# Kernel optimization log

Hardware: AMD Instinct MI355X
Metric: run time of the kernel (lower is better)

Reference implementation:

```python
import jax, jax.numpy as jnp
import numpy as np

KN = 4        # kernel_number
K = 3         # kernel size
CIN = 256
COUT = 256
BN_EPS = 1e-5


def _rotation_matrices(thetas):
    """thetas: [b, n] -> rot mats [b, n, 9, 9] (faithful port of _get_rotation_matrix)."""
    b, n = thetas.shape
    t = thetas.reshape(-1)                      # [b*n]
    x = jnp.cos(t); y = jnp.sin(t)
    a = x - y; bxy = x * y; c = x + y
    z = jnp.zeros_like(t); o = jnp.ones_like(t)
    pos = [
        [a, 1 - a, z, z, z, z, z, z, z],
        [z, x - bxy, bxy, z, 1 - c + bxy, y - bxy, z, z, z],
        [z, z, a, z, z, 1 - a, z, z, z],
        [bxy, y - bxy, z, x - bxy, 1 - c + bxy, z, z, z, z],
        [z, z, z, z, o, z, z, z, z],
        [z, z, z, z, 1 - c + bxy, x - bxy, z, y - bxy, bxy],
        [z, z, z, 1 - a, z, z, a, z, z],
        [z, z, z, y - bxy, 1 - c + bxy, z, bxy, x - bxy, z],
        [z, z, z, z, z, z, z, 1 - a, a],
    ]
    neg = [
        [c, z, z, 1 - c, z, z, z, z, z],
        [-bxy, x + bxy, z, bxy - y, 1 - a - bxy, z, z, z, z],
        [z, 1 - c, c, z, z, z, z, z, z],
        [z, z, z, x + bxy, 1 - a - bxy, z, -bxy, bxy - y, z],
        [z, z, z, z, o, z, z, z, z],
        [z, bxy - y, -bxy, z, 1 - a - bxy, x + bxy, z, z, z],
        [z, z, z, z, z, z, c, 1 - c, z],
        [z, z, z, z, 1 - a - bxy, bxy - y, z, x + bxy, -bxy],
        [z, z, z, z, z, 1 - c, z, z, c],
    ]
    P = jnp.stack([jnp.stack(r, 0) for r in pos], 0)    # [9, 9, b*n]
    N = jnp.stack([jnp.stack(r, 0) for r in neg], 0)    # [9, 9, b*n]
    R = jnp.where(t >= 0, P, N)                          # [9, 9, b*n]
    return R.transpose(2, 0, 1).reshape(b, n, K * K, K * K)


def _rotate_weights(weights, lambdas, thetas):
    """weights [n, Cout, Cin, 3, 3], lambdas/thetas [b, n] -> [b*Cout, Cin, 3, 3]."""
    b, n = thetas.shape
    _, Cout, Cin, _, _ = weights.shape
    rot = _rotation_matrices(thetas) * lambdas[:, :, None, None]   # [b, n, 9, 9]
    rot = rot.transpose(0, 2, 1, 3).reshape(b * K * K, n * K * K)  # [b*9, n*9]
    w = weights.transpose(0, 3, 4, 1, 2).reshape(n * K * K, Cout * Cin)
    w = rot @ w                                                    # [b*9, Cout*Cin]
    w = w.reshape(b, K, K, Cout, Cin).transpose(0, 3, 4, 1, 2)
    return w.reshape(b * Cout, Cin, K, K)


def _forward(x, weight, w_lambda, w_theta, bn_gamma, bn_beta, bn_mean, bn_var):
    b, Cin, H, W = x.shape
    Cout = weight.shape[1]
    # routing: GAP -> linear heads (sigmoid for lambdas, softsign*pi for thetas)
    pooled = x.mean(axis=(2, 3))                        # [b, Cin]
    lambdas = jax.nn.sigmoid(pooled @ w_lambda)         # [b, n]
    thetas = jax.nn.soft_sign(pooled @ w_theta) * jnp.pi  # [b, n]
    # per-sample rotated weights + grouped conv (groups = b)
    rw = _rotate_weights(weight, lambdas, thetas)       # [b*Cout, Cin, 3, 3]
    xr = x.reshape(1, b * Cin, H, W)
    out = jax.lax.conv_general_dilated(
        xr, rw, window_strides=(1, 1), padding=((1, 1), (1, 1)),
        dimension_numbers=('NCHW', 'OIHW', 'NCHW'), feature_group_count=b)
    out = out.reshape(b, Cout, H, W)
    # BatchNorm (inference, running stats) + ReLU
    inv = jax.lax.rsqrt(bn_var + BN_EPS)
    out = (out - bn_mean[None, :, None, None]) * (inv * bn_gamma)[None, :, None, None] \
          + bn_beta[None, :, None, None]
    return jax.nn.relu(out)


def setup_inputs() -> dict:
    key = jax.random.key(0)
    ks = jax.random.split(key, 8)
    B, H, W = 16, 64, 64
    x = jax.random.normal(ks[0], (B, CIN, H, W), dtype=jnp.float32)
    fan_in = CIN * K * K
    weight = jax.random.normal(ks[1], (KN, COUT, CIN, K, K), dtype=jnp.float32) * np.sqrt(2.0 / fan_in)
    w_lambda = jax.random.normal(ks[2], (CIN, KN), dtype=jnp.float32) * np.sqrt(2.0 / CIN)
    w_theta = jax.random.normal(ks[3], (CIN, KN), dtype=jnp.float32) * np.sqrt(2.0 / CIN)
    bn_gamma = jax.random.uniform(ks[4], (COUT,), dtype=jnp.float32, minval=0.5, maxval=1.5)
    bn_beta = jax.random.normal(ks[5], (COUT,), dtype=jnp.float32) * 0.1
    bn_mean = jax.random.normal(ks[6], (COUT,), dtype=jnp.float32) * 0.1
    bn_var = jax.random.uniform(ks[7], (COUT,), dtype=jnp.float32, minval=0.5, maxval=1.5)
    return {'x': x, 'weight': weight, 'w_lambda': w_lambda, 'w_theta': w_theta,
            'bn_gamma': bn_gamma, 'bn_beta': bn_beta, 'bn_mean': bn_mean, 'bn_var': bn_var}


def reference(x, weight, w_lambda, w_theta, bn_gamma, bn_beta, bn_mean, bn_var):
    return _forward(x, weight, w_lambda, w_theta, bn_gamma, bn_beta, bn_mean, bn_var)
```

## Files before the change

### kernel.cpp

```cpp
#include <hip/hip_runtime.h>
#include <math.h>

typedef __bf16  bf16x8 __attribute__((ext_vector_type(8)));
typedef float   f32x4  __attribute__((ext_vector_type(4)));

#define GLD_LDS16(dst, src)                                                      \
    __builtin_amdgcn_global_load_lds(                                            \
        (const __attribute__((address_space(1))) unsigned int*)(src),            \
        (__attribute__((address_space(3))) unsigned int*)(dst), 16, 0, 0)

__global__ __launch_bounds__(256) void transpose_kernel(const float* __restrict__ x,
                                                        __bf16* __restrict__ xT) {
    int h = blockIdx.x, b = blockIdx.y;
    int lane = threadIdx.x & 63, wv = threadIdx.x >> 6;
#pragma unroll
    for (int i = 0; i < 8; i++) {
        int cq = i * 4 + wv;
        const float* src = x + (((size_t)(b * 256 + cq * 8) * 64 + h) * 64 + lane);
        bf16x8 o;
#pragma unroll
        for (int j = 0; j < 8; j++) o[j] = (__bf16)src[(size_t)j * 4096];
        *(bf16x8*)(xT + (((size_t)(b * 64 + h) * 64 + lane) * 256 + cq * 8)) = o;
    }
}

__global__ __launch_bounds__(256) void pool_kernel(const float* __restrict__ x,
                                                   float* __restrict__ pooled) {
    int bc = blockIdx.x;
    const float* p = x + (size_t)bc * 4096;
    int t = threadIdx.x;
    float s = 0.f;
#pragma unroll
    for (int i = 0; i < 16; i++) s += p[t + i * 256];
#pragma unroll
    for (int off = 32; off > 0; off >>= 1) s += __shfl_down(s, off, 64);
    __shared__ float red[4];
    if ((t & 63) == 0) red[t >> 6] = s;
    __syncthreads();
    if (t == 0) pooled[bc] = (red[0] + red[1] + red[2] + red[3]) * (1.f / 4096.f);
}

__global__ __launch_bounds__(256) void rotw_kernel(
    const float* __restrict__ weight, const float* __restrict__ pooled,
    const float* __restrict__ w_lambda, const float* __restrict__ w_theta,
    __bf16* __restrict__ rwq) {
    __shared__ __attribute__((aligned(16))) float sl[16][4][9][12];
    __shared__ float wlds[4][2304];
    int co = blockIdx.x;
    int t = threadIdx.x;
#pragma unroll
    for (int n = 0; n < 4; n++) {
        const float* wp = weight + ((size_t)n * 256 + co) * 2304;
        for (int i = t; i < 2304; i += 256) wlds[n][i] = wp[i];
    }
    if (t < 64) {
        int b = t >> 2, n = t & 3;
        float zl = 0.f, zt = 0.f;
        for (int ci = 0; ci < 256; ci++) {
            float p = pooled[b * 256 + ci];
            zl += p * w_lambda[ci * 4 + n];
            zt += p * w_theta[ci * 4 + n];
        }
        float lam = 1.f / (1.f + expf(-zl));
        float th  = 3.14159265358979323846f * (zt / (1.f + fabsf(zt)));
        float xc = cosf(th), ys = sinf(th);
        float a = xc - ys, bb = xc * ys, c = xc + ys;
        float R[9][9];
#pragma unroll
        for (int i = 0; i < 9; i++)
#pragma unroll
            for (int j = 0; j < 9; j++) R[i][j] = 0.f;
        if (th >= 0.f) {
            R[0][0] = a;       R[0][1] = 1 - a;
            R[1][1] = xc - bb; R[1][2] = bb;       R[1][4] = 1 - c + bb; R[1][5] = ys - bb;
            R[2][2] = a;       R[2][5] = 1 - a;
            R[3][0] = bb;      R[3][1] = ys - bb;  R[3][3] = xc - bb;    R[3][4] = 1 - c + bb;
            R[4][4] = 1.f;
            R[5][4] = 1 - c + bb; R[5][5] = xc - bb; R[5][7] = ys - bb;  R[5][8] = bb;
            R[6][3] = 1 - a;   R[6][6] = a;
            R[7][3] = ys - bb; R[7][4] = 1 - c + bb; R[7][6] = bb;       R[7][7] = xc - bb;
            R[8][7] = 1 - a;   R[8][8] = a;
        } else {
            R[0][0] = c;       R[0][3] = 1 - c;
            R[1][0] = -bb;     R[1][1] = xc + bb;  R[1][3] = bb - ys;    R[1][4] = 1 - a - bb;
            R[2][1] = 1 - c;   R[2][2] = c;
            R[3][3] = xc + bb; R[3][4] = 1 - a - bb; R[3][6] = -bb;      R[3][7] = bb - ys;
            R[4][4] = 1.f;
            R[5][1] = bb - ys; R[5][2] = -bb;      R[5][4] = 1 - a - bb; R[5][5] = xc + bb;
            R[6][6] = c;       R[6][7] = 1 - c;
            R[7][4] = 1 - a - bb; R[7][5] = bb - ys; R[7][7] = xc + bb;  R[7][8] = -bb;
            R[8][5] = 1 - c;   R[8][8] = c;
        }
#pragma unroll
        for (int p = 0; p < 9; p++) {
#pragma unroll
            for (int q = 0; q < 9; q++) sl[b][n][p][q] = lam * R[p][q];
            sl[b][n][p][9] = sl[b][n][p][10] = sl[b][n][p][11] = 0.f;
        }
    }
    __syncthreads();
    int ci = t;
    float4 wa[4], wb[4];
    float  wc[4];
#pragma unroll
    for (int n = 0; n < 4; n++) {
        const float* wp = &wlds[n][ci * 9];
        wa[n] = make_float4(wp[0], wp[1], wp[2], wp[3]);
        wb[n] = make_float4(wp[4], wp[5], wp[6], wp[7]);
        wc[n] = wp[8];
    }
    for (int b = 0; b < 16; b++) {
#pragma unroll
        for (int p = 0; p < 9; p++) {
            float s = 0.f;
#pragma unroll
            for (int n = 0; n < 4; n++) {
                float4 sa = *(const float4*)&sl[b][n][p][0];
                float4 sb = *(const float4*)&sl[b][n][p][4];
                float  sc = sl[b][n][p][8];
                s += sa.x * wa[n].x + sa.y * wa[n].y + sa.z * wa[n].z + sa.w * wa[n].w
                   + sb.x * wb[n].x + sb.y * wb[n].y + sb.z * wb[n].z + sb.w * wb[n].w
                   + sc * wc[n];
            }
            rwq[(((size_t)b * 9 + p) * 256 + co) * 256 + ci] = (__bf16)s;
        }
    }
}

__global__ __launch_bounds__(256, 2) void conv_kernel(
    const __bf16* __restrict__ xT, const __bf16* __restrict__ rwq,
    const float* __restrict__ bn_gamma, const float* __restrict__ bn_beta,
    const float* __restrict__ bn_mean,  const float* __restrict__ bn_var,
    float* __restrict__ out) {
    __shared__ __attribute__((aligned(16))) __bf16 xs[10][4][66][8];
    __shared__ __attribute__((aligned(16))) __bf16 as9[9][4][66][8];
    __shared__ float bns[64], bnh[64];

    const int t    = threadIdx.x;
    const int lane = t & 63;
    const int wv   = t >> 6;
    const int l15  = lane & 15;
    const int kq4  = lane >> 4;

    const int lin  = blockIdx.x;
    const int r    = lin & 7;
    const int k    = lin >> 3;
    const int b    = (r << 1) | (k >> 5);
    const int inner = k & 31;
    const int co0  = (inner & 3) << 6;
    const int h0   = (inner >> 2) << 3;

    if (t < 64) {
        float inv = rsqrtf(bn_var[co0 + t] + 1e-5f);
        float sc = bn_gamma[co0 + t] * inv;
        bns[t] = sc;
        bnh[t] = bn_beta[co0 + t] - bn_mean[co0 + t] * sc;
    }

    f32x4 acc[2][4][4];
#pragma unroll
    for (int rr = 0; rr < 2; rr++)
#pragma unroll
        for (int m = 0; m < 4; m++)
#pragma unroll
            for (int n = 0; n < 4; n++) acc[rr][m][n] = (f32x4){0.f, 0.f, 0.f, 0.f};

    const uint4 zero4 = {0u, 0u, 0u, 0u};
    if (t < 40) {
        int rr = t >> 2, kq = t & 3;
        *(uint4*)&xs[rr][kq][0][0]  = zero4;
        *(uint4*)&xs[rr][kq][65][0] = zero4;
    }

    for (int ci0 = 0; ci0 < 256; ci0 += 32) {
        __syncthreads();
#pragma unroll
        for (int u = wv * 10; u < wv * 10 + 10; u++) {
            int rr = u >> 2, kq = u & 3;
            int hh = h0 - 1 + rr;
            if (hh >= 0 && hh < 64) {
                const __bf16* src = xT + (((size_t)(b * 64 + hh) * 64 + lane) * 256 + ci0 + kq * 8);
                GLD_LDS16(&xs[rr][kq][1 + lane][0], src);
            } else {
                *(uint4*)&xs[rr][kq][1 + lane][0] = zero4;
            }
        }
#pragma unroll
        for (int u = wv * 9; u < wv * 9 + 9; u++) {
            int tap = u >> 2, kq = u & 3;
            const __bf16* src = rwq +
                ((((size_t)b * 9 + tap) * 256 + co0 + lane) * 256 + ci0 + kq * 8);
            GLD_LDS16(&as9[tap][kq][lane][0], src);
        }
        __syncthreads();
#pragma unroll
        for (int tap = 0; tap < 9; tap++) {
            const int dh = tap / 3, dw = tap % 3;
            bf16x8 af[4];
#pragma unroll
            for (int m = 0; m < 4; m++)
                af[m] = *(const bf16x8*)&as9[tap][kq4][m * 16 + l15][0];
#pragma unroll
            for (int rr = 0; rr < 2; rr++) {
                const int hl = wv + rr * 4;
#pragma unroll
                for (int nt = 0; nt < 4; nt++) {
                    bf16x8 bfr = *(const bf16x8*)&xs[hl + dh][kq4][nt * 16 + l15 + dw][0];
#pragma unroll
                    for (int m = 0; m < 4; m++)
                        acc[rr][m][nt] = __builtin_amdgcn_mfma_f32_16x16x32_bf16(
                            af[m], bfr, acc[rr][m][nt], 0, 0, 0);
                }
            }
        }
    }

#pragma unroll
    for (int rr = 0; rr < 2; rr++) {
        const int h = h0 + wv + rr * 4;
#pragma unroll
        for (int m = 0; m < 4; m++) {
#pragma unroll
            for (int reg = 0; reg < 4; reg++) {
                int col = m * 16 + kq4 * 4 + reg;
                float sc = bns[col], sh = bnh[col];
                int co = co0 + col;
#pragma unroll
                for (int nt = 0; nt < 4; nt++) {
                    int w = nt * 16 + l15;
                    float v = acc[rr][m][nt][reg] * sc + sh;
                    out[(((size_t)b * 256 + co) * 64 + h) * 64 + w] = v > 0.f ? v : 0.f;
                }
            }
        }
    }
}

extern "C" void kernel_launch(void* const* d_in, const int* in_sizes, int n_in,
                              void* d_out, int out_size, void* d_ws, size_t ws_size,
                              hipStream_t stream) {
    const float* x        = (const float*)d_in[0];
    const float* weight   = (const float*)d_in[1];
    const float* w_lambda = (const float*)d_in[2];
    const float* w_theta  = (const float*)d_in[3];
    const float* bn_gamma = (const float*)d_in[4];
    const float* bn_beta  = (const float*)d_in[5];
    const float* bn_mean  = (const float*)d_in[6];
    const float* bn_var   = (const float*)d_in[7];
    float* out = (float*)d_out;

    char* ws = (char*)d_ws;
    float*  pooled  = (float*)(ws);
    __bf16* xT      = (__bf16*)(ws + 49152);
    __bf16* rwq     = (__bf16*)(ws + 49152 + 33554432);

    transpose_kernel<<<dim3(64, 16), 256, 0, stream>>>(x, xT);
    pool_kernel<<<4096, 256, 0, stream>>>(x, pooled);
    rotw_kernel<<<256, 256, 0, stream>>>(weight, pooled, w_lambda, w_theta, rwq);
    conv_kernel<<<512, 256, 0, stream>>>(xT, rwq,
                                         bn_gamma, bn_beta, bn_mean, bn_var, out);
}
```

Before: 269.0 us.

## Double-buffer conv input tiles, load weights from global, pool from bf16 transpose

The conv kernel now uses 512-thread blocks covering 16 output rows and double-buffers the input tile in LDS, prefetching the next channel chunk while computing. Weight fragments are read straight from global memory instead of being staged in LDS. Pooling reads the smaller bf16 transposed tensor and reduces with atomics, with zeroing done in the transpose kernel. The risks are more global weight traffic per tap, pooled means computed from bf16-rounded inputs, and halving the grid to one block per CU.

```diff
diff --git a/kernel.cpp b/kernel.cpp
--- a/kernel.cpp
+++ b/kernel.cpp
@@ -10,7 +10,11 @@
         (__attribute__((address_space(3))) unsigned int*)(dst), 16, 0, 0)
 
 __global__ __launch_bounds__(256) void transpose_kernel(const float* __restrict__ x,
-                                                        __bf16* __restrict__ xT) {
+                                                        __bf16* __restrict__ xT,
+                                                        float* __restrict__ pooled) {
+    if (blockIdx.x == 0 && blockIdx.y == 0) {
+        for (int i = threadIdx.x; i < 4096; i += 256) pooled[i] = 0.f;
+    }
     int h = blockIdx.x, b = blockIdx.y;
     int lane = threadIdx.x & 63, wv = threadIdx.x >> 6;
 #pragma unroll
@@ -24,20 +28,36 @@
     }
 }
 
-__global__ __launch_bounds__(256) void pool_kernel(const float* __restrict__ x,
+__global__ __launch_bounds__(256) void pool_kernel(const __bf16* __restrict__ xT,
                                                    float* __restrict__ pooled) {
-    int bc = blockIdx.x;
-    const float* p = x + (size_t)bc * 4096;
+    int blk = blockIdx.x;
+    int b = blk >> 4, s = blk & 15;
     int t = threadIdx.x;
-    float s = 0.f;
-#pragma unroll
-    for (int i = 0; i < 16; i++) s += p[t + i * 256];
-#pragma unroll
-    for (int off = 32; off > 0; off >>= 1) s += __shfl_down(s, off, 64);
-    __shared__ float red[4];
-    if ((t & 63) == 0) red[t >> 6] = s;
+    int oc  = (t & 31) << 3;
+    int hw0 = t >> 5;
+    float a8[8];
+#pragma unroll
+    for (int j = 0; j < 8; j++) a8[j] = 0.f;
+    const __bf16* base = xT + (((size_t)b * 4096 + s * 256 + hw0) * 256) + oc;
+#pragma unroll 4
+    for (int i = 0; i < 32; ++i) {
+        bf16x8 v = *(const bf16x8*)(base + (size_t)i * 8 * 256);
+#pragma unroll
+        for (int j = 0; j < 8; j++) a8[j] += (float)v[j];
+    }
+    __shared__ float red[256][8];
+#pragma unroll
+    for (int j = 0; j < 8; j++) red[t][j] = a8[j];
     __syncthreads();
-    if (t == 0) pooled[bc] = (red[0] + red[1] + red[2] + red[3]) * (1.f / 4096.f);
+    if (t < 32) {
+#pragma unroll
+        for (int j = 0; j < 8; j++) {
+            float s8 = 0.f;
+#pragma unroll
+            for (int g = 0; g < 8; g++) s8 += red[g * 32 + t][j];
+            atomicAdd(&pooled[b * 256 + t * 8 + j], s8 * (1.f / 4096.f));
+        }
+    }
 }
 
 __global__ __launch_bounds__(256) void rotw_kernel(
@@ -127,13 +147,26 @@
     }
 }
 
-__global__ __launch_bounds__(256, 2) void conv_kernel(
+#define STAGE_X(bufsel, ci0_)                                                     \
+    _Pragma("unroll")                                                             \
+    for (int u = wv * 9; u < wv * 9 + 9; ++u) {                                   \
+        int rr_ = u >> 2, kq_ = u & 3;                                            \
+        int hh_ = h0 - 1 + rr_;                                                   \
+        if (hh_ >= 0 && hh_ < 64) {                                               \
+            const __bf16* src_ = xT + (((size_t)(b * 64 + hh_) * 64 + lane) * 256 \
+                                       + (ci0_) + kq_ * 8);                       \
+            GLD_LDS16(&xs[bufsel][rr_][kq_][1 + lane][0], src_);                  \
+        } else {                                                                  \
+            *(uint4*)&xs[bufsel][rr_][kq_][1 + lane][0] = zero4;                  \
+        }                                                                         \
+    }
+
+__global__ __launch_bounds__(512) void conv_kernel(
     const __bf16* __restrict__ xT, const __bf16* __restrict__ rwq,
     const float* __restrict__ bn_gamma, const float* __restrict__ bn_beta,
     const float* __restrict__ bn_mean,  const float* __restrict__ bn_var,
     float* __restrict__ out) {
-    __shared__ __attribute__((aligned(16))) __bf16 xs[10][4][66][8];
-    __shared__ __attribute__((aligned(16))) __bf16 as9[9][4][66][8];
+    __shared__ __attribute__((aligned(16))) __bf16 xs[2][18][4][66][8];
     __shared__ float bns[64], bnh[64];
 
     const int t    = threadIdx.x;
@@ -145,10 +178,10 @@
     const int lin  = blockIdx.x;
     const int r    = lin & 7;
     const int k    = lin >> 3;
-    const int b    = (r << 1) | (k >> 5);
-    const int inner = k & 31;
+    const int b    = (r << 1) | (k >> 4);
+    const int inner = k & 15;
     const int co0  = (inner & 3) << 6;
-    const int h0   = (inner >> 2) << 3;
+    const int h0   = (inner >> 2) << 4;
 
     if (t < 64) {
         float inv = rsqrtf(bn_var[co0 + t] + 1e-5f);
@@ -157,6 +190,16 @@
         bnh[t] = bn_beta[co0 + t] - bn_mean[co0 + t] * sc;
     }
 
+    const uint4 zero4 = {0u, 0u, 0u, 0u};
+    if (t < 288) {
+        int side = t & 1;
+        int kq = (t >> 1) & 3;
+        int rem = t >> 3;
+        int rr = rem % 18;
+        int bf = rem / 18;
+        *(uint4*)&xs[bf][rr][kq][side * 65][0] = zero4;
+    }
+
     f32x4 acc[2][4][4];
 #pragma unroll
     for (int rr = 0; rr < 2; rr++)
@@ -165,47 +208,28 @@
 #pragma unroll
             for (int n = 0; n < 4; n++) acc[rr][m][n] = (f32x4){0.f, 0.f, 0.f, 0.f};
 
-    const uint4 zero4 = {0u, 0u, 0u, 0u};
-    if (t < 40) {
-        int rr = t >> 2, kq = t & 3;
-        *(uint4*)&xs[rr][kq][0][0]  = zero4;
-        *(uint4*)&xs[rr][kq][65][0] = zero4;
-    }
-
-    for (int ci0 = 0; ci0 < 256; ci0 += 32) {
-        __syncthreads();
-#pragma unroll
-        for (int u = wv * 10; u < wv * 10 + 10; u++) {
-            int rr = u >> 2, kq = u & 3;
-            int hh = h0 - 1 + rr;
-            if (hh >= 0 && hh < 64) {
-                const __bf16* src = xT + (((size_t)(b * 64 + hh) * 64 + lane) * 256 + ci0 + kq * 8);
-                GLD_LDS16(&xs[rr][kq][1 + lane][0], src);
-            } else {
-                *(uint4*)&xs[rr][kq][1 + lane][0] = zero4;
-            }
-        }
-#pragma unroll
-        for (int u = wv * 9; u < wv * 9 + 9; u++) {
-            int tap = u >> 2, kq = u & 3;
-            const __bf16* src = rwq +
-                ((((size_t)b * 9 + tap) * 256 + co0 + lane) * 256 + ci0 + kq * 8);
-            GLD_LDS16(&as9[tap][kq][lane][0], src);
-        }
-        __syncthreads();
+    STAGE_X(0, 0);
+    __syncthreads();
+
+    for (int c = 0; c < 8; ++c) {
+        const int cur = c & 1;
+        const int ci0 = c << 5;
+        if (c < 7) { STAGE_X(cur ^ 1, ci0 + 32); }
 #pragma unroll
         for (int tap = 0; tap < 9; tap++) {
             const int dh = tap / 3, dw = tap % 3;
             bf16x8 af[4];
 #pragma unroll
             for (int m = 0; m < 4; m++)
-                af[m] = *(const bf16x8*)&as9[tap][kq4][m * 16 + l15][0];
+                af[m] = *(const bf16x8*)(rwq +
+                    ((((size_t)b * 9 + tap) * 256 + co0 + m * 16 + l15) * 256
+                     + ci0 + kq4 * 8));
 #pragma unroll
             for (int rr = 0; rr < 2; rr++) {
-                const int hl = wv + rr * 4;
+                const int hl = wv * 2 + rr;
 #pragma unroll
                 for (int nt = 0; nt < 4; nt++) {
-                    bf16x8 bfr = *(const bf16x8*)&xs[hl + dh][kq4][nt * 16 + l15 + dw][0];
+                    bf16x8 bfr = *(const bf16x8*)&xs[cur][hl + dh][kq4][nt * 16 + l15 + dw][0];
 #pragma unroll
                     for (int m = 0; m < 4; m++)
                         acc[rr][m][nt] = __builtin_amdgcn_mfma_f32_16x16x32_bf16(
@@ -213,11 +237,12 @@
                 }
             }
         }
+        __syncthreads();
     }
 
 #pragma unroll
     for (int rr = 0; rr < 2; rr++) {
-        const int h = h0 + wv + rr * 4;
+        const int h = h0 + wv * 2 + rr;
 #pragma unroll
         for (int m = 0; m < 4; m++) {
 #pragma unroll
@@ -254,9 +279,9 @@
     __bf16* xT      = (__bf16*)(ws + 49152);
     __bf16* rwq     = (__bf16*)(ws + 49152 + 33554432);
 
-    transpose_kernel<<<dim3(64, 16), 256, 0, stream>>>(x, xT);
-    pool_kernel<<<4096, 256, 0, stream>>>(x, pooled);
+    transpose_kernel<<<dim3(64, 16), 256, 0, stream>>>(x, xT, pooled);
+    pool_kernel<<<256, 256, 0, stream>>>(xT, pooled);
     rotw_kernel<<<256, 256, 0, stream>>>(weight, pooled, w_lambda, w_theta, rwq);
-    conv_kernel<<<512, 256, 0, stream>>>(xT, rwq,
+    conv_kernel<<<256, 512, 0, stream>>>(xT, rwq,
                                          bn_gamma, bn_beta, bn_mean, bn_var, out);
 }
```

Result: slower. 343.0 us (+27.5%).

## Stage transpose through LDS, pool from bf16 copy, hoist routing into own kernel

Applied to the files above, without the earlier changes.

The transpose kernel now reads x with coalesced float4 loads, packs channel pairs into LDS and writes contiguous 16-byte chunks of xT. The pool kernel now reduces the half-size bf16 xT instead of rereading the fp32 input, and accumulates into pooled with atomics after the transpose kernel zeroes it. The routing computation (lambda/theta and the rotation matrices) moves into a single small kernel, so the 256 rotw blocks no longer each recompute it serially. The aim is to cut global memory traffic and redundant serial work. The cost is pooling from bf16-rounded values, plus one extra launch and atomics.

```diff
diff --git a/kernel.cpp b/kernel.cpp
--- a/kernel.cpp
+++ b/kernel.cpp
@@ -10,39 +10,128 @@
         (__attribute__((address_space(3))) unsigned int*)(dst), 16, 0, 0)
 
 __global__ __launch_bounds__(256) void transpose_kernel(const float* __restrict__ x,
-                                                        __bf16* __restrict__ xT) {
-    int h = blockIdx.x, b = blockIdx.y;
-    int lane = threadIdx.x & 63, wv = threadIdx.x >> 6;
-#pragma unroll
-    for (int i = 0; i < 8; i++) {
-        int cq = i * 4 + wv;
-        const float* src = x + (((size_t)(b * 256 + cq * 8) * 64 + h) * 64 + lane);
-        bf16x8 o;
-#pragma unroll
-        for (int j = 0; j < 8; j++) o[j] = (__bf16)src[(size_t)j * 4096];
-        *(bf16x8*)(xT + (((size_t)(b * 64 + h) * 64 + lane) * 256 + cq * 8)) = o;
-    }
-}
-
-__global__ __launch_bounds__(256) void pool_kernel(const float* __restrict__ x,
+                                                        __bf16* __restrict__ xT,
+                                                        float* __restrict__ pooled) {
+    __shared__ unsigned int lp[128][68];
+    const int h = blockIdx.x, b = blockIdx.y;
+    const int t = threadIdx.x;
+    if (h == 0 && b == 0) {
+        for (int i = t; i < 4096; i += 256) pooled[i] = 0.f;
+    }
+    const int w4 = t & 15;
+#pragma unroll
+    for (int k = 0; k < 8; ++k) {
+        int ci2 = k * 16 + (t >> 4);
+        int ci  = ci2 * 2;
+        const float4 a = *(const float4*)(x + (((size_t)(b * 256 + ci    ) * 64 + h) * 64 + w4 * 4));
+        const float4 c = *(const float4*)(x + (((size_t)(b * 256 + ci + 1) * 64 + h) * 64 + w4 * 4));
+        union { __bf16 hh[2]; unsigned int u; } p0, p1, p2, p3;
+        p0.hh[0] = (__bf16)a.x; p0.hh[1] = (__bf16)c.x;
+        p1.hh[0] = (__bf16)a.y; p1.hh[1] = (__bf16)c.y;
+        p2.hh[0] = (__bf16)a.z; p2.hh[1] = (__bf16)c.z;
+        p3.hh[0] = (__bf16)a.w; p3.hh[1] = (__bf16)c.w;
+        uint4 v = {p0.u, p1.u, p2.u, p3.u};
+        *(uint4*)&lp[ci2][w4 * 4] = v;
+    }
+    __syncthreads();
+    const int w = t >> 2, q = t & 3;
+    __bf16* dst = xT + (((size_t)b * 64 + h) * 64 + w) * 256 + q * 64;
+#pragma unroll
+    for (int j = 0; j < 8; ++j) {
+        int c0 = q * 32 + j * 4;
+        uint4 v;
+        v.x = lp[c0 + 0][w];
+        v.y = lp[c0 + 1][w];
+        v.z = lp[c0 + 2][w];
+        v.w = lp[c0 + 3][w];
+        *(uint4*)(dst + j * 8) = v;
+    }
+}
+
+__global__ __launch_bounds__(256) void pool_kernel(const __bf16* __restrict__ xT,
                                                    float* __restrict__ pooled) {
-    int bc = blockIdx.x;
-    const float* p = x + (size_t)bc * 4096;
+    int blk = blockIdx.x;
+    int b = blk >> 4, s = blk & 15;
     int t = threadIdx.x;
-    float s = 0.f;
-#pragma unroll
-    for (int i = 0; i < 16; i++) s += p[t + i * 256];
-#pragma unroll
-    for (int off = 32; off > 0; off >>= 1) s += __shfl_down(s, off, 64);
-    __shared__ float red[4];
-    if ((t & 63) == 0) red[t >> 6] = s;
+    int oc  = (t & 31) << 3;
+    int hw0 = t >> 5;
+    float a8[8];
+#pragma unroll
+    for (int j = 0; j < 8; j++) a8[j] = 0.f;
+    const __bf16* base = xT + (((size_t)b * 4096 + s * 256 + hw0) * 256) + oc;
+#pragma unroll 4
+    for (int i = 0; i < 32; ++i) {
+        bf16x8 v = *(const bf16x8*)(base + (size_t)i * 8 * 256);
+#pragma unroll
+        for (int j = 0; j < 8; j++) a8[j] += (float)v[j];
+    }
+    __shared__ float red[256][8];
+#pragma unroll
+    for (int j = 0; j < 8; j++) red[t][j] = a8[j];
     __syncthreads();
-    if (t == 0) pooled[bc] = (red[0] + red[1] + red[2] + red[3]) * (1.f / 4096.f);
+    if (t < 32) {
+#pragma unroll
+        for (int j = 0; j < 8; j++) {
+            float s8 = 0.f;
+#pragma unroll
+            for (int g = 0; g < 8; g++) s8 += red[g * 32 + t][j];
+            atomicAdd(&pooled[b * 256 + t * 8 + j], s8 * (1.f / 4096.f));
+        }
+    }
+}
+
+__global__ __launch_bounds__(64) void routing_kernel(
+    const float* __restrict__ pooled, const float* __restrict__ w_lambda,
+    const float* __restrict__ w_theta, float* __restrict__ slg) {
+    int t = threadIdx.x;
+    int b = t >> 2, n = t & 3;
+    float zl = 0.f, zt = 0.f;
+    for (int ci = 0; ci < 256; ci++) {
+        float p = pooled[b * 256 + ci];
+        zl += p * w_lambda[ci * 4 + n];
+        zt += p * w_theta[ci * 4 + n];
+    }
+    float lam = 1.f / (1.f + expf(-zl));
+    float th  = 3.14159265358979323846f * (zt / (1.f + fabsf(zt)));
+    float xc = cosf(th), ys = sinf(th);
+    float a = xc - ys, bb = xc * ys, c = xc + ys;
+    float R[9][9];
+#pragma unroll
+    for (int i = 0; i < 9; i++)
+#pragma unroll
+        for (int j = 0; j < 9; j++) R[i][j] = 0.f;
+    if (th >= 0.f) {
+        R[0][0] = a;       R[0][1] = 1 - a;
+        R[1][1] = xc - bb; R[1][2] = bb;       R[1][4] = 1 - c + bb; R[1][5] = ys - bb;
+        R[2][2] = a;       R[2][5] = 1 - a;
+        R[3][0] = bb;      R[3][1] = ys - bb;  R[3][3] = xc - bb;    R[3][4] = 1 - c + bb;
+        R[4][4] = 1.f;
+        R[5][4] = 1 - c + bb; R[5][5] = xc - bb; R[5][7] = ys - bb;  R[5][8] = bb;
+        R[6][3] = 1 - a;   R[6][6] = a;
+        R[7][3] = ys - bb; R[7][4] = 1 - c + bb; R[7][6] = bb;       R[7][7] = xc - bb;
+        R[8][7] = 1 - a;   R[8][8] = a;
+    } else {
+        R[0][0] = c;       R[0][3] = 1 - c;
+        R[1][0] = -bb;     R[1][1] = xc + bb;  R[1][3] = bb - ys;    R[1][4] = 1 - a - bb;
+        R[2][1] = 1 - c;   R[2][2] = c;
+        R[3][3] = xc + bb; R[3][4] = 1 - a - bb; R[3][6] = -bb;      R[3][7] = bb - ys;
+        R[4][4] = 1.f;
+        R[5][1] = bb - ys; R[5][2] = -bb;      R[5][4] = 1 - a - bb; R[5][5] = xc + bb;
+        R[6][6] = c;       R[6][7] = 1 - c;
+        R[7][4] = 1 - a - bb; R[7][5] = bb - ys; R[7][7] = xc + bb;  R[7][8] = -bb;
+        R[8][5] = 1 - c;   R[8][8] = c;
+    }
+    float* o = slg + ((size_t)(b * 4 + n) * 9) * 12;
+#pragma unroll
+    for (int p = 0; p < 9; p++) {
+#pragma unroll
+        for (int q = 0; q < 9; q++) o[p * 12 + q] = lam * R[p][q];
+        o[p * 12 + 9] = o[p * 12 + 10] = o[p * 12 + 11] = 0.f;
+    }
 }
 
 __global__ __launch_bounds__(256) void rotw_kernel(
-    const float* __restrict__ weight, const float* __restrict__ pooled,
-    const float* __restrict__ w_lambda, const float* __restrict__ w_theta,
+    const float* __restrict__ weight, const float* __restrict__ slg,
     __bf16* __restrict__ rwq) {
     __shared__ __attribute__((aligned(16))) float sl[16][4][9][12];
     __shared__ float wlds[4][2304];
@@ -53,51 +142,8 @@
         const float* wp = weight + ((size_t)n * 256 + co) * 2304;
         for (int i = t; i < 2304; i += 256) wlds[n][i] = wp[i];
     }
-    if (t < 64) {
-        int b = t >> 2, n = t & 3;
-        float zl = 0.f, zt = 0.f;
-        for (int ci = 0; ci < 256; ci++) {
-            float p = pooled[b * 256 + ci];
-            zl += p * w_lambda[ci * 4 + n];
-            zt += p * w_theta[ci * 4 + n];
-        }
-        float lam = 1.f / (1.f + expf(-zl));
-        float th  = 3.14159265358979323846f * (zt / (1.f + fabsf(zt)));
-        float xc = cosf(th), ys = sinf(th);
-        float a = xc - ys, bb = xc * ys, c = xc + ys;
-        float R[9][9];
-#pragma unroll
-        for (int i = 0; i < 9; i++)
-#pragma unroll
-            for (int j = 0; j < 9; j++) R[i][j] = 0.f;
-        if (th >= 0.f) {
-            R[0][0] = a;       R[0][1] = 1 - a;
-            R[1][1] = xc - bb; R[1][2] = bb;       R[1][4] = 1 - c + bb; R[1][5] = ys - bb;
-            R[2][2] = a;       R[2][5] = 1 - a;
-            R[3][0] = bb;      R[3][1] = ys - bb;  R[3][3] = xc - bb;    R[3][4] = 1 - c + bb;
-            R[4][4] = 1.f;
-            R[5][4] = 1 - c + bb; R[5][5] = xc - bb; R[5][7] = ys - bb;  R[5][8] = bb;
-            R[6][3] = 1 - a;   R[6][6] = a;
-            R[7][3] = ys - bb; R[7][4] = 1 - c + bb; R[7][6] = bb;       R[7][7] = xc - bb;
-            R[8][7] = 1 - a;   R[8][8] = a;
-        } else {
-            R[0][0] = c;       R[0][3] = 1 - c;
-            R[1][0] = -bb;     R[1][1] = xc + bb;  R[1][3] = bb - ys;    R[1][4] = 1 - a - bb;
-            R[2][1] = 1 - c;   R[2][2] = c;
-            R[3][3] = xc + bb; R[3][4] = 1 - a - bb; R[3][6] = -bb;      R[3][7] = bb - ys;
-            R[4][4] = 1.f;
-            R[5][1] = bb - ys; R[5][2] = -bb;      R[5][4] = 1 - a - bb; R[5][5] = xc + bb;
-            R[6][6] = c;       R[6][7] = 1 - c;
-            R[7][4] = 1 - a - bb; R[7][5] = bb - ys; R[7][7] = xc + bb;  R[7][8] = -bb;
-            R[8][5] = 1 - c;   R[8][8] = c;
-        }
-#pragma unroll
-        for (int p = 0; p < 9; p++) {
-#pragma unroll
-            for (int q = 0; q < 9; q++) sl[b][n][p][q] = lam * R[p][q];
-            sl[b][n][p][9] = sl[b][n][p][10] = sl[b][n][p][11] = 0.f;
-        }
-    }
+    for (int i = t; i < 1728; i += 256)
+        ((float4*)sl)[i] = ((const float4*)slg)[i];
     __syncthreads();
     int ci = t;
     float4 wa[4], wb[4];
@@ -251,12 +297,14 @@
 
     char* ws = (char*)d_ws;
     float*  pooled  = (float*)(ws);
+    float*  slg     = (float*)(ws + 16384);
     __bf16* xT      = (__bf16*)(ws + 49152);
     __bf16* rwq     = (__bf16*)(ws + 49152 + 33554432);
 
-    transpose_kernel<<<dim3(64, 16), 256, 0, stream>>>(x, xT);
-    pool_kernel<<<4096, 256, 0, stream>>>(x, pooled);
-    rotw_kernel<<<256, 256, 0, stream>>>(weight, pooled, w_lambda, w_theta, rwq);
+    transpose_kernel<<<dim3(64, 16), 256, 0, stream>>>(x, xT, pooled);
+    pool_kernel<<<256, 256, 0, stream>>>(xT, pooled);
+    routing_kernel<<<1, 64, 0, stream>>>(pooled, w_lambda, w_theta, slg);
+    rotw_kernel<<<256, 256, 0, stream>>>(weight, slg, rwq);
     conv_kernel<<<512, 256, 0, stream>>>(xT, rwq,
                                          bn_gamma, bn_beta, bn_mean, bn_var, out);
 }
```

Measured after the change: 268.4 us. No clear change (-0.2%).
